# Performance work log

Measured on AMD Instinct MI355X. Metric: run time of the kernel, lower is better.

Reference implementation:

```python
import jax, jax.numpy as jnp
import numpy as np
import math

H = 1024      # hidden_size
NH = 16       # num_attention_heads
HD = H // NH  # head_dim = 64
FF = 4096     # intermediate_size
AD = 256      # adapter_hidden_size
NB = 320      # num_buckets
MAXD = 800    # max_bucket_distance
B = 4
S = 1024
EPS = 1e-5


def _rel_bucket(rel):
    # HF WavLM _relative_positions_bucket
    nb = NB // 2
    buckets = (rel > 0).astype(jnp.int32) * nb
    rel = jnp.abs(rel)
    max_exact = nb // 2
    is_small = rel < max_exact
    large = max_exact + (
        jnp.log(jnp.maximum(rel, 1).astype(jnp.float32) / max_exact)
        / math.log(MAXD / max_exact) * (nb - max_exact)
    ).astype(jnp.int32)
    large = jnp.minimum(large, nb - 1)
    return buckets + jnp.where(is_small, rel, large)


def _ln(x, g, b):
    m = x.mean(-1, keepdims=True)
    v = ((x - m) ** 2).mean(-1, keepdims=True)
    return (x - m) * jax.lax.rsqrt(v + EPS) * g + b


def setup_inputs() -> dict:
    key = jax.random.key(0)
    ks = jax.random.split(key, 12)
    sc = 0.02
    w = lambda k, shape: jax.random.normal(k, shape, jnp.float32) * sc
    return dict(
        x=jax.random.normal(ks[0], (B, S, H), jnp.float32),
        Wq=w(ks[1], (H, H)), bq=jnp.zeros((H,), jnp.float32),
        Wk=w(ks[2], (H, H)), bk=jnp.zeros((H,), jnp.float32),
        Wv=w(ks[3], (H, H)), bv=jnp.zeros((H,), jnp.float32),
        Wo=w(ks[4], (H, H)), bo=jnp.zeros((H,), jnp.float32),
        Wg=w(ks[5], (8, HD)), bg=jnp.zeros((8,), jnp.float32),
        gru_const=jnp.ones((1, NH, 1, 1), jnp.float32),
        rel_embed=w(ks[6], (NB, NH)),
        ln1_g=jnp.ones((H,), jnp.float32), ln1_b=jnp.zeros((H,), jnp.float32),
        W1=w(ks[7], (FF, H)), b1=jnp.zeros((FF,), jnp.float32),
        W2=w(ks[8], (H, FF)), b2=jnp.zeros((H,), jnp.float32),
        ln2_g=jnp.ones((H,), jnp.float32), ln2_b=jnp.zeros((H,), jnp.float32),
        Wad=w(ks[9], (AD, H)), bad=jnp.zeros((AD,), jnp.float32),
        Wau=w(ks[10], (H, AD)), bau=jnp.zeros((H,), jnp.float32),
    )


def reference(x, Wq, bq, Wk, bk, Wv, bv, Wo, bo, Wg, bg, gru_const, rel_embed,
              ln1_g, ln1_b, W1, b1, W2, b2, ln2_g, ln2_b, Wad, bad, Wau, bau):
    b, s, _ = x.shape
    # --- relative position bias (first layer: position_bias=None) ---
    pos = jnp.arange(s)
    rel = pos[None, :] - pos[:, None]                 # memory - context
    pos_bias = rel_embed[_rel_bucket(rel)].transpose(2, 0, 1)  # (nh, s, s)

    # --- GRU-style gating of the bias (per batch, head, query pos) ---
    xh = x.reshape(b, s, NH, HD).transpose(0, 2, 1, 3)         # (b, nh, s, hd)
    gproj = jnp.einsum('bhsd,ed->bhse', xh, Wg) + bg           # (b, nh, s, 8)
    gproj = gproj.reshape(b, NH, s, 2, 4).sum(-1)              # (b, nh, s, 2)
    gate = jax.nn.sigmoid(gproj)
    gate_a, gate_b = gate[..., 0:1], gate[..., 1:2]            # (b, nh, s, 1)
    gate_out = gate_a * (gate_b * gru_const - 1.0) + 2.0       # (b, nh, s, 1)
    gated_bias = gate_out * pos_bias[None]                     # (b, nh, s, s)

    # --- multi-head self-attention with additive gated bias ---
    q = (x @ Wq.T + bq).reshape(b, s, NH, HD)
    k = (x @ Wk.T + bk).reshape(b, s, NH, HD)
    v = (x @ Wv.T + bv).reshape(b, s, NH, HD)
    scores = jnp.einsum('bihd,bjhd->bhij', q, k) * (HD ** -0.5) + gated_bias
    attn = jax.nn.softmax(scores, axis=-1)
    ctx = jnp.einsum('bhij,bjhd->bihd', attn, v).reshape(b, s, H)
    attn_out = ctx @ Wo.T + bo

    # --- residual + LN, FFN + adapter (idx_without_adapter=None path) + LN ---
    h = _ln(x + attn_out, ln1_g, ln1_b)
    ff = jax.nn.gelu(h @ W1.T + b1, approximate=False) @ W2.T + b2
    adapt = jax.nn.elu(h @ Wad.T + bad) @ Wau.T + bau
    h = h + ff + adapt
    return _ln(h, ln2_g, ln2_b)
```

## Files before the change

### kernel.cpp

```cpp
#include <hip/hip_runtime.h>
#include <cmath>

typedef unsigned short u16;
using short8 = __attribute__((ext_vector_type(8))) short;
using f32x4  = __attribute__((ext_vector_type(4))) float;

__device__ __forceinline__ u16 f2bf(float f) {
  union { float f; unsigned u; } c; c.f = f;
  unsigned r = c.u + 0x7fffu + ((c.u >> 16) & 1u);
  return (u16)(r >> 16);
}
__device__ __forceinline__ float bf2f(u16 b) {
  union { unsigned u; float f; } c; c.u = ((unsigned)b) << 16;
  return c.f;
}

__device__ __forceinline__ void gld_lds16(void* lds, const void* g) {
  __builtin_amdgcn_global_load_lds(
      (const __attribute__((address_space(1))) void*)g,
      (__attribute__((address_space(3))) void*)lds, 16, 0, 0);
}

__global__ __launch_bounds__(256) void cvt_bf16(const float* __restrict__ in,
                                                u16* __restrict__ out, int n4) {
  int i = blockIdx.x * 256 + threadIdx.x;
  if (i >= n4) return;
  float4 v = ((const float4*)in)[i];
  ushort4 o;
  o.x = f2bf(v.x); o.y = f2bf(v.y); o.z = f2bf(v.z); o.w = f2bf(v.w);
  ((ushort4*)out)[i] = o;
}

__global__ __launch_bounds__(256) void btab_kernel(const float* __restrict__ rel_embed,
                                                   float* __restrict__ btab) {
  int idx = blockIdx.x * 256 + threadIdx.x;
  if (idx >= 16 * 2048) return;
  int h = idx >> 11;
  int d = idx & 2047;
  if (d >= 2047) return;
  int rel = d - 1023;
  int bucket = (rel > 0) ? 160 : 0;
  int ar = rel < 0 ? -rel : rel;
  if (ar < 80) {
    bucket += ar;
  } else {
    int large = 80 + (int)(logf((float)ar / 80.0f) / 2.3025851f * 80.0f);
    if (large > 159) large = 159;
    bucket += large;
  }
  btab[h * 2048 + d] = rel_embed[bucket * 16 + h];
}

__global__ __launch_bounds__(256) void gate_kernel(const float* __restrict__ x,
                                                   const float* __restrict__ Wg,
                                                   const float* __restrict__ bg,
                                                   const float* __restrict__ gc,
                                                   float* __restrict__ gate_out) {
  int gw = blockIdx.x * 4 + (threadIdx.x >> 6);
  int lane = threadIdx.x & 63;
  int s = gw & 1023, bh = gw >> 10, b = bh >> 4, h = bh & 15;
  float wA = Wg[lane] + Wg[64 + lane] + Wg[128 + lane] + Wg[192 + lane];
  float wB = Wg[256 + lane] + Wg[320 + lane] + Wg[384 + lane] + Wg[448 + lane];
  float xv = x[((size_t)(b * 1024 + s)) * 1024 + h * 64 + lane];
  float pa = xv * wA, pb = xv * wB;
  #pragma unroll
  for (int m = 1; m < 64; m <<= 1) {
    pa += __shfl_xor(pa, m, 64);
    pb += __shfl_xor(pb, m, 64);
  }
  if (lane == 0) {
    float bgA = bg[0] + bg[1] + bg[2] + bg[3];
    float bgB = bg[4] + bg[5] + bg[6] + bg[7];
    float ga = 1.f / (1.f + expf(-(pa + bgA)));
    float gb = 1.f / (1.f + expf(-(pb + bgB)));
    gate_out[(size_t)bh * 1024 + s] = ga * (gb * gc[h] - 1.f) + 2.f;
  }
}

__global__ __launch_bounds__(256) void vtrans_kernel(const u16* __restrict__ vb,
                                                     u16* __restrict__ vt) {
  __shared__ u16 tile[64 * 65];
  int bh = blockIdx.y, b = bh >> 4, h = bh & 15;
  int s0 = blockIdx.x * 64;
  int tid = threadIdx.x;
  int r = tid >> 3, c = (tid & 7) * 8;
  #pragma unroll
  for (int p = 0; p < 2; ++p) {
    int s = p * 32 + r;
    uint4 vv = *(const uint4*)&vb[((size_t)(b * 1024 + s0 + s)) * 1024 + h * 64 + c];
    const u16* pv = (const u16*)&vv;
    #pragma unroll
    for (int e = 0; e < 8; ++e) tile[(c + e) * 65 + s] = pv[e];
  }
  __syncthreads();
  int d = tid & 63, jc0 = tid >> 6;
  #pragma unroll
  for (int jc = jc0; jc < 8; jc += 4) {
    u16 tmp[8];
    #pragma unroll
    for (int e = 0; e < 8; ++e) tmp[e] = tile[d * 65 + jc * 8 + e];
    *(uint4*)&vt[((size_t)(bh * 64 + d)) * 1024 + s0 + jc * 8] = *(uint4*)tmp;
  }
}

template <int MODE>
__global__ __launch_bounds__(256, 3) void gemm_bt(
    const u16* __restrict__ A, const u16* __restrict__ Bw,
    int Kfull, int Ksub, int N,
    const float* __restrict__ bias0, const float* __restrict__ bias1,
    const float* __restrict__ bias2,
    float* __restrict__ outf, float* __restrict__ outf1,
    u16* __restrict__ ob0, u16* __restrict__ ob1, u16* __restrict__ ob2) {
  __shared__ __align__(16) u16 As[2][128 * 32];
  __shared__ __align__(16) u16 Bs[2][128 * 32];
  const int tid = threadIdx.x;
  const int lane = tid & 63, wave = tid >> 6;
  const int quad = lane >> 4, l16 = lane & 15;
  const int bm = blockIdx.x * 128, bn = blockIdx.y * 128;
  const int kz = blockIdx.z;
  const int k0base = kz * Ksub;
  const int nsteps = Ksub >> 5;
  const int wm = (wave & 1) * 64, wn = (wave >> 1) * 64;
  const int sr = lane & 15;
  const int skc = (lane >> 4) * 8;

  const u16* a0 = A + (size_t)(bm + wave * 32 + sr) * Kfull + k0base + skc;
  const u16* b0 = Bw + (size_t)(bn + wave * 32 + sr) * Kfull + k0base + skc;
  const size_t rstep = (size_t)16 * Kfull;

  f32x4 acc[4][4] = {};

  gld_lds16(&As[0][wave * 1024], a0);
  gld_lds16(&As[0][wave * 1024 + 512], a0 + rstep);
  gld_lds16(&Bs[0][wave * 1024], b0);
  gld_lds16(&Bs[0][wave * 1024 + 512], b0 + rstep);

  int p = 0;
  for (int ks = 0; ks < nsteps; ++ks) {
    if (ks + 1 < nsteps) {
      int ko = (ks + 1) * 32;
      gld_lds16(&As[p ^ 1][wave * 1024], a0 + ko);
      gld_lds16(&As[p ^ 1][wave * 1024 + 512], a0 + rstep + ko);
      gld_lds16(&Bs[p ^ 1][wave * 1024], b0 + ko);
      gld_lds16(&Bs[p ^ 1][wave * 1024 + 512], b0 + rstep + ko);
      asm volatile("s_waitcnt vmcnt(4)" ::: "memory");
    } else {
      asm volatile("s_waitcnt vmcnt(0)" ::: "memory");
    }
    __builtin_amdgcn_s_barrier();

    const u16* Ap = As[p];
    const u16* Bp = Bs[p];
    short8 af[4], bf[4];
    #pragma unroll
    for (int mi = 0; mi < 4; ++mi)
      af[mi] = *(const short8*)&Ap[((wm >> 4) + mi) * 512 + quad * 128 + l16 * 8];
    #pragma unroll
    for (int ni = 0; ni < 4; ++ni)
      bf[ni] = *(const short8*)&Bp[((wn >> 4) + ni) * 512 + quad * 128 + l16 * 8];
    #pragma unroll
    for (int mi = 0; mi < 4; ++mi)
      #pragma unroll
      for (int ni = 0; ni < 4; ++ni)
        acc[mi][ni] = __builtin_amdgcn_mfma_f32_16x16x32_bf16(af[mi], bf[ni], acc[mi][ni], 0, 0, 0);

    __builtin_amdgcn_s_barrier();
    p ^= 1;
  }

  float* outp = (MODE == 3) ? (kz ? outf1 : outf) : outf;

  #pragma unroll
  for (int mi = 0; mi < 4; ++mi) {
    #pragma unroll
    for (int ni = 0; ni < 4; ++ni) {
      int col = bn + wn + ni * 16 + l16;
      #pragma unroll
      for (int r = 0; r < 4; ++r) {
        int m = bm + wm + mi * 16 + quad * 4 + r;
        float v = acc[mi][ni][r];
        if constexpr (MODE == 0) {
          int seg = col >> 10;
          int nloc = col & 1023;
          const float* bs = seg == 0 ? bias0 : (seg == 1 ? bias1 : bias2);
          u16* dst = seg == 0 ? ob0 : (seg == 1 ? ob1 : ob2);
          v += bs[nloc];
          if (seg == 0) v *= 0.125f;
          dst[(size_t)m * 1024 + nloc] = f2bf(v);
        } else if constexpr (MODE == 2) {
          if (col < 4096) {
            float t = v + bias0[col];
            float g = 0.5f * t * (1.f + erff(t * 0.70710678118f));
            ob0[(size_t)m * 4096 + col] = f2bf(g);
          } else {
            int nloc = col - 4096;
            float t = v + bias1[nloc];
            float e = t > 0.f ? t : expm1f(t);
            ob1[(size_t)m * 256 + nloc] = f2bf(e);
          }
        } else if constexpr (MODE == 3) {
          outp[(size_t)m * N + col] = v;
        } else {
          outp[(size_t)m * N + col] += v;
        }
      }
    }
  }
}

__global__ __launch_bounds__(256) void attn_kernel(
    const u16* __restrict__ qb, const u16* __restrict__ kb, const u16* __restrict__ vt,
    const float* __restrict__ gate, const float* __restrict__ btab,
    u16* __restrict__ ctxb) {
  __shared__ __align__(16) u16 Qs[64 * 64];
  __shared__ __align__(16) u16 Ks[64 * 64];
  __shared__ __align__(16) u16 Vs[64 * 64];
  __shared__ __align__(16) u16 Ps[4][16 * 64];
  __shared__ u16 btl[2048];
  __shared__ float gbuf[64];

  const int tid = threadIdx.x;
  const int lane = tid & 63, wave = tid >> 6;
  const int quad = lane >> 4, l16 = lane & 15;
  const int it0 = blockIdx.x * 64;
  const int bh = blockIdx.y, b = bh >> 4, h = bh & 15;
  const int sr = lane & 15;
  const int skc = (lane >> 4) * 8;

  for (int idx = tid; idx < 2047; idx += 256) btl[idx] = f2bf(btab[h * 2048 + idx]);
  if (tid < 64) gbuf[tid] = gate[(size_t)bh * 1024 + it0 + tid];

  #pragma unroll
  for (int hf = 0; hf < 2; ++hf)
    gld_lds16(&Qs[wave * 1024 + hf * 512],
              &qb[((size_t)(b * 1024 + it0 + wave * 16 + sr)) * 1024 + h * 64 + hf * 32 + skc]);

  f32x4 oacc[4] = {};
  float mrow[4], lrow[4];
  #pragma unroll
  for (int r = 0; r < 4; ++r) { mrow[r] = -1e30f; lrow[r] = 0.f; }

  __syncthreads();

  for (int jt = 0; jt < 16; ++jt) {
    int j0 = jt * 64;
    #pragma unroll
    for (int hf = 0; hf < 2; ++hf) {
      gld_lds16(&Ks[wave * 1024 + hf * 512],
                &kb[((size_t)(b * 1024 + j0 + wave * 16 + sr)) * 1024 + h * 64 + hf * 32 + skc]);
      gld_lds16(&Vs[wave * 1024 + hf * 512],
                &vt[((size_t)(bh * 64 + wave * 16 + sr)) * 1024 + j0 + hf * 32 + skc]);
    }
    __syncthreads();

    f32x4 sacc[4] = {};
    #pragma unroll
    for (int c = 0; c < 2; ++c) {
      short8 aq = *(const short8*)&Qs[wave * 1024 + (c * 4 + quad) * 128 + l16 * 8];
      #pragma unroll
      for (int nt = 0; nt < 4; ++nt) {
        short8 bk8 = *(const short8*)&Ks[nt * 1024 + (c * 4 + quad) * 128 + l16 * 8];
        sacc[nt] = __builtin_amdgcn_mfma_f32_16x16x32_bf16(aq, bk8, sacc[nt], 0, 0, 0);
      }
    }

    float sc[4][4], mt[4];
    #pragma unroll
    for (int r = 0; r < 4; ++r) {
      int i_loc = wave * 16 + quad * 4 + r;
      int i_glob = it0 + i_loc;
      float g = gbuf[i_loc];
      float mx = -1e30f;
      #pragma unroll
      for (int nt = 0; nt < 4; ++nt) {
        int j = j0 + nt * 16 + l16;
        float s = sacc[nt][r] + g * bf2f(btl[j - i_glob + 1023]);
        sc[nt][r] = s;
        mx = fmaxf(mx, s);
      }
      mt[r] = mx;
    }
    #pragma unroll
    for (int m = 1; m < 16; m <<= 1)
      #pragma unroll
      for (int r = 0; r < 4; ++r) mt[r] = fmaxf(mt[r], __shfl_xor(mt[r], m, 64));

    float alpha[4], ls[4];
    #pragma unroll
    for (int r = 0; r < 4; ++r) {
      float mnew = fmaxf(mrow[r], mt[r]);
      alpha[r] = __expf(mrow[r] - mnew);
      mrow[r] = mnew;
      float lsum = 0.f;
      #pragma unroll
      for (int nt = 0; nt < 4; ++nt) {
        float p = __expf(sc[nt][r] - mnew);
        sc[nt][r] = p;
        lsum += p;
      }
      ls[r] = lsum;
    }
    #pragma unroll
    for (int m = 1; m < 16; m <<= 1)
      #pragma unroll
      for (int r = 0; r < 4; ++r) ls[r] += __shfl_xor(ls[r], m, 64);
    #pragma unroll
    for (int r = 0; r < 4; ++r) lrow[r] = lrow[r] * alpha[r] + ls[r];

    #pragma unroll
    for (int nt = 0; nt < 4; ++nt)
      #pragma unroll
      for (int r = 0; r < 4; ++r)
        Ps[wave][(nt * 2 + (l16 >> 3)) * 128 + (quad * 4 + r) * 8 + (l16 & 7)] = f2bf(sc[nt][r]);

    #pragma unroll
    for (int dt = 0; dt < 4; ++dt)
      #pragma unroll
      for (int r = 0; r < 4; ++r) oacc[dt][r] *= alpha[r];

    #pragma unroll
    for (int c = 0; c < 2; ++c) {
      short8 ap = *(const short8*)&Ps[wave][(c * 4 + quad) * 128 + l16 * 8];
      #pragma unroll
      for (int dt = 0; dt < 4; ++dt) {
        short8 bv8 = *(const short8*)&Vs[dt * 1024 + (c * 4 + quad) * 128 + l16 * 8];
        oacc[dt] = __builtin_amdgcn_mfma_f32_16x16x32_bf16(ap, bv8, oacc[dt], 0, 0, 0);
      }
    }
    __syncthreads();
  }

  #pragma unroll
  for (int dt = 0; dt < 4; ++dt)
    #pragma unroll
    for (int r = 0; r < 4; ++r) {
      int i_loc = wave * 16 + quad * 4 + r;
      int d = dt * 16 + l16;
      float o = oacc[dt][r] / lrow[r];
      ctxb[((size_t)(b * 1024 + it0 + i_loc)) * 1024 + h * 64 + d] = f2bf(o);
    }
}

template <bool WRITE_BF16, bool TWO_BIAS>
__global__ __launch_bounds__(256) void redln_kernel(
    const float* __restrict__ p0, const float* __restrict__ p1,
    const float* __restrict__ extra, const float* __restrict__ bias,
    const float* __restrict__ bias2,
    const float* __restrict__ g, const float* __restrict__ bta,
    float* __restrict__ outf, u16* __restrict__ outb) {
  __shared__ float red[8];
  int row = blockIdx.x, tid = threadIdx.x;
  int lane = tid & 63, wave = tid >> 6;
  size_t base = (size_t)row * 1024 + tid * 4;
  float4 a = *(const float4*)&p0[base];
  float4 bb = *(const float4*)&p1[base];
  float4 c = *(const float4*)&extra[base];
  float4 d = *(const float4*)&bias[tid * 4];
  float4 v;
  v.x = a.x + bb.x + c.x + d.x;
  v.y = a.y + bb.y + c.y + d.y;
  v.z = a.z + bb.z + c.z + d.z;
  v.w = a.w + bb.w + c.w + d.w;
  if (TWO_BIAS) {
    float4 d2 = *(const float4*)&bias2[tid * 4];
    v.x += d2.x; v.y += d2.y; v.z += d2.z; v.w += d2.w;
  }
  float s = v.x + v.y + v.z + v.w;
  #pragma unroll
  for (int m = 1; m < 64; m <<= 1) s += __shfl_xor(s, m, 64);
  if (lane == 0) red[wave] = s;
  __syncthreads();
  float mean = (red[0] + red[1] + red[2] + red[3]) * (1.f / 1024.f);
  float d0 = v.x - mean, d1 = v.y - mean, d2 = v.z - mean, d3 = v.w - mean;
  float sq = d0 * d0 + d1 * d1 + d2 * d2 + d3 * d3;
  #pragma unroll
  for (int m = 1; m < 64; m <<= 1) sq += __shfl_xor(sq, m, 64);
  if (lane == 0) red[4 + wave] = sq;
  __syncthreads();
  float var = (red[4] + red[5] + red[6] + red[7]) * (1.f / 1024.f);
  float rstd = rsqrtf(var + 1e-5f);
  float dd[4] = {d0, d1, d2, d3};
  #pragma unroll
  for (int e = 0; e < 4; ++e) {
    int cidx = tid * 4 + e;
    float val = dd[e] * rstd * g[cidx] + bta[cidx];
    outf[(size_t)row * 1024 + cidx] = val;
    if (WRITE_BF16) outb[(size_t)row * 1024 + cidx] = f2bf(val);
  }
}

extern "C" void kernel_launch(void* const* d_in, const int* in_sizes, int n_in,
                              void* d_out, int out_size, void* d_ws, size_t ws_size,
                              hipStream_t stream) {
  const float* x    = (const float*)d_in[0];
  const float* Wq   = (const float*)d_in[1];  const float* bq  = (const float*)d_in[2];
  const float* Wk   = (const float*)d_in[3];  const float* bk  = (const float*)d_in[4];
  const float* Wv   = (const float*)d_in[5];  const float* bv  = (const float*)d_in[6];
  const float* Wo   = (const float*)d_in[7];  const float* bo  = (const float*)d_in[8];
  const float* Wg   = (const float*)d_in[9];  const float* bg  = (const float*)d_in[10];
  const float* gc   = (const float*)d_in[11];
  const float* rel  = (const float*)d_in[12];
  const float* ln1g = (const float*)d_in[13]; const float* ln1b = (const float*)d_in[14];
  const float* W1   = (const float*)d_in[15]; const float* b1  = (const float*)d_in[16];
  const float* W2   = (const float*)d_in[17]; const float* b2  = (const float*)d_in[18];
  const float* ln2g = (const float*)d_in[19]; const float* ln2b = (const float*)d_in[20];
  const float* Wad  = (const float*)d_in[21]; const float* bad = (const float*)d_in[22];
  const float* Wau  = (const float*)d_in[23]; const float* bau = (const float*)d_in[24];
  float* out = (float*)d_out;

  char* ws = (char*)d_ws;
  const size_t MB = 1ull << 20;
  const size_t KB = 1ull << 10;
  u16*   xb   = (u16*)(ws + 0 * MB);
  u16*   wqkv = (u16*)(ws + 8 * MB);
  u16*   w1ad = (u16*)(ws + 16 * MB);
  u16*   w2b  = (u16*)(ws + 25 * MB);
  u16*   waub = (u16*)(ws + 33 * MB);
  u16*   wob  = (u16*)(ws + 34 * MB);
  u16*   qb   = (u16*)(ws + 36 * MB);
  u16*   kb   = (u16*)(ws + 44 * MB);
  u16*   vbp  = (u16*)(ws + 52 * MB);
  float* gate = (float*)(ws + 60 * MB);
  float* btab = (float*)(ws + 60 * MB + 256 * KB);
  u16*   ctxb = (u16*)(ws + 61 * MB);
  u16*   vtb  = (u16*)(ws + 69 * MB);
  float* hf   = (float*)(ws + 77 * MB);
  u16*   hb   = (u16*)(ws + 93 * MB);
  float* wop0 = (float*)(ws + 0 * MB);
  float* wop1 = (float*)(ws + 101 * MB);
  u16*   ffb  = (u16*)(ws + 36 * MB);
  u16*   adp  = (u16*)(ws + 68 * MB);
  float* p0   = (float*)(ws + 0 * MB);
  float* p1   = (float*)(ws + 101 * MB);
  (void)ws_size; (void)n_in; (void)in_sizes; (void)out_size;

  auto cvt = [&](const float* src, u16* dst, int n) {
    cvt_bf16<<<(n / 4 + 255) / 256, 256, 0, stream>>>(src, dst, n / 4);
  };
  cvt(x, xb, 4096 * 1024);
  cvt(Wq, wqkv,               1024 * 1024);
  cvt(Wk, wqkv + 1024 * 1024, 1024 * 1024);
  cvt(Wv, wqkv + 2 * 1024 * 1024, 1024 * 1024);
  cvt(Wo, wob, 1024 * 1024);
  cvt(W1, w1ad, 4096 * 1024);
  cvt(Wad, w1ad + 4096 * 1024, 256 * 1024);
  cvt(W2, w2b, 4096 * 1024);
  cvt(Wau, waub, 1024 * 256);

  btab_kernel<<<128, 256, 0, stream>>>(rel, btab);
  gate_kernel<<<16384, 256, 0, stream>>>(x, Wg, bg, gc, gate);

  gemm_bt<0><<<dim3(32, 24, 1), 256, 0, stream>>>(xb, wqkv, 1024, 1024, 3072,
      bq, bk, bv, nullptr, nullptr, qb, kb, vbp);
  vtrans_kernel<<<dim3(16, 64), 256, 0, stream>>>(vbp, vtb);
  attn_kernel<<<dim3(16, 64), 256, 0, stream>>>(qb, kb, vtb, gate, btab, ctxb);
  gemm_bt<3><<<dim3(32, 8, 2), 256, 0, stream>>>(ctxb, wob, 1024, 512, 1024,
      nullptr, nullptr, nullptr, wop0, wop1, nullptr, nullptr, nullptr);
  redln_kernel<true, false><<<4096, 256, 0, stream>>>(wop0, wop1, x, bo, nullptr,
      ln1g, ln1b, hf, hb);
  gemm_bt<2><<<dim3(32, 34, 1), 256, 0, stream>>>(hb, w1ad, 1024, 1024, 4352,
      b1, bad, nullptr, nullptr, nullptr, ffb, adp, nullptr);
  gemm_bt<3><<<dim3(32, 8, 2), 256, 0, stream>>>(ffb, w2b, 4096, 2048, 1024,
      nullptr, nullptr, nullptr, p0, p1, nullptr, nullptr, nullptr);
  gemm_bt<4><<<dim3(32, 8, 1), 256, 0, stream>>>(adp, waub, 256, 256, 1024,
      nullptr, nullptr, nullptr, p0, nullptr, nullptr, nullptr, nullptr);
  redln_kernel<false, true><<<4096, 256, 0, stream>>>(p0, p1, hf, b2, bau,
      ln2g, ln2b, out, nullptr);
}
```

Baseline: 570.5 us.

## Use 256x128 GEMM tiles with triple-buffered LDS and fuse adapter-up into FFN-down

The bf16 MFMA GEMM now uses 256x128 block tiles, with each wave computing 128x64, and a three-stage LDS pipeline that prefetches two k-steps ahead. It also drops the second barrier per iteration. The FFN-down GEMM and adapter-up GEMM are merged into one K=4352 GEMM by concatenating the GELU and ELU activations and padding W2 and Wau into one interleaved weight matrix, which removes a separate accumulate pass. Larger tiles raise arithmetic intensity but halve the grid, lower occupancy to two blocks per CU and need more registers and LDS.

```diff
diff --git a/kernel.cpp b/kernel.cpp
--- a/kernel.cpp
+++ b/kernel.cpp
@@ -29,6 +29,18 @@
   ushort4 o;
   o.x = f2bf(v.x); o.y = f2bf(v.y); o.z = f2bf(v.z); o.w = f2bf(v.w);
   ((ushort4*)out)[i] = o;
+}
+
+__global__ __launch_bounds__(256) void cvt_pad(const float* __restrict__ in,
+                                               u16* __restrict__ out,
+                                               int incols4, int outstride, int n4) {
+  int i = blockIdx.x * 256 + threadIdx.x;
+  if (i >= n4) return;
+  int row = i / incols4, c = i - row * incols4;
+  float4 v = ((const float4*)in)[i];
+  ushort4 o;
+  o.x = f2bf(v.x); o.y = f2bf(v.y); o.z = f2bf(v.z); o.w = f2bf(v.w);
+  *(ushort4*)&out[(size_t)row * outstride + c * 4] = o;
 }
 
 __global__ __launch_bounds__(256) void btab_kernel(const float* __restrict__ rel_embed,
@@ -104,80 +116,80 @@
 }
 
 template <int MODE>
-__global__ __launch_bounds__(256, 3) void gemm_bt(
+__global__ __launch_bounds__(256, 2) void gemm_bt(
     const u16* __restrict__ A, const u16* __restrict__ Bw,
-    int Kfull, int Ksub, int N,
+    int K, int Ksub, int N,
     const float* __restrict__ bias0, const float* __restrict__ bias1,
     const float* __restrict__ bias2,
-    float* __restrict__ outf, float* __restrict__ outf1,
+    float* __restrict__ outf,
     u16* __restrict__ ob0, u16* __restrict__ ob1, u16* __restrict__ ob2) {
-  __shared__ __align__(16) u16 As[2][128 * 32];
-  __shared__ __align__(16) u16 Bs[2][128 * 32];
+  __shared__ __align__(16) u16 As[3][256 * 32];
+  __shared__ __align__(16) u16 Bs[3][128 * 32];
   const int tid = threadIdx.x;
   const int lane = tid & 63, wave = tid >> 6;
   const int quad = lane >> 4, l16 = lane & 15;
-  const int bm = blockIdx.x * 128, bn = blockIdx.y * 128;
+  const int bm = blockIdx.x * 256, bn = blockIdx.y * 128;
   const int kz = blockIdx.z;
-  const int k0base = kz * Ksub;
   const int nsteps = Ksub >> 5;
-  const int wm = (wave & 1) * 64, wn = (wave >> 1) * 64;
-  const int sr = lane & 15;
-  const int skc = (lane >> 4) * 8;
-
-  const u16* a0 = A + (size_t)(bm + wave * 32 + sr) * Kfull + k0base + skc;
-  const u16* b0 = Bw + (size_t)(bn + wave * 32 + sr) * Kfull + k0base + skc;
-  const size_t rstep = (size_t)16 * Kfull;
-
-  f32x4 acc[4][4] = {};
-
-  gld_lds16(&As[0][wave * 1024], a0);
-  gld_lds16(&As[0][wave * 1024 + 512], a0 + rstep);
-  gld_lds16(&Bs[0][wave * 1024], b0);
-  gld_lds16(&Bs[0][wave * 1024 + 512], b0 + rstep);
-
-  int p = 0;
+  const int sr = lane & 15, skc = (lane >> 4) * 8;
+
+  const u16* a0 = A + (size_t)(bm + wave * 64 + sr) * K + kz * Ksub + skc;
+  const u16* b0 = Bw + (size_t)(bn + wave * 32 + sr) * K + kz * Ksub + skc;
+  const size_t ra = (size_t)16 * K;
+
+  f32x4 acc[8][4] = {};
+
+  #pragma unroll
+  for (int t = 0; t < 4; ++t) gld_lds16(&As[0][(wave * 4 + t) * 512], a0 + t * ra);
+  #pragma unroll
+  for (int t = 0; t < 2; ++t) gld_lds16(&Bs[0][(wave * 2 + t) * 512], b0 + t * ra);
+  if (nsteps > 1) {
+    #pragma unroll
+    for (int t = 0; t < 4; ++t) gld_lds16(&As[1][(wave * 4 + t) * 512], a0 + t * ra + 32);
+    #pragma unroll
+    for (int t = 0; t < 2; ++t) gld_lds16(&Bs[1][(wave * 2 + t) * 512], b0 + t * ra + 32);
+  }
+
+  int cur = 0, nxt2 = 2;
   for (int ks = 0; ks < nsteps; ++ks) {
-    if (ks + 1 < nsteps) {
-      int ko = (ks + 1) * 32;
-      gld_lds16(&As[p ^ 1][wave * 1024], a0 + ko);
-      gld_lds16(&As[p ^ 1][wave * 1024 + 512], a0 + rstep + ko);
-      gld_lds16(&Bs[p ^ 1][wave * 1024], b0 + ko);
-      gld_lds16(&Bs[p ^ 1][wave * 1024 + 512], b0 + rstep + ko);
-      asm volatile("s_waitcnt vmcnt(4)" ::: "memory");
-    } else {
-      asm volatile("s_waitcnt vmcnt(0)" ::: "memory");
-    }
+    if (ks + 1 < nsteps) asm volatile("s_waitcnt vmcnt(6)" ::: "memory");
+    else                 asm volatile("s_waitcnt vmcnt(0)" ::: "memory");
     __builtin_amdgcn_s_barrier();
-
-    const u16* Ap = As[p];
-    const u16* Bp = Bs[p];
-    short8 af[4], bf[4];
-    #pragma unroll
-    for (int mi = 0; mi < 4; ++mi)
-      af[mi] = *(const short8*)&Ap[((wm >> 4) + mi) * 512 + quad * 128 + l16 * 8];
+    if (ks + 2 < nsteps) {
+      int ko = (ks + 2) * 32;
+      #pragma unroll
+      for (int t = 0; t < 4; ++t) gld_lds16(&As[nxt2][(wave * 4 + t) * 512], a0 + t * ra + ko);
+      #pragma unroll
+      for (int t = 0; t < 2; ++t) gld_lds16(&Bs[nxt2][(wave * 2 + t) * 512], b0 + t * ra + ko);
+    }
+    const u16* Ap = As[cur];
+    const u16* Bp = Bs[cur];
+    short8 af[8], bf[4];
+    #pragma unroll
+    for (int mi = 0; mi < 8; ++mi)
+      af[mi] = *(const short8*)&Ap[((wave & 1) * 8 + mi) * 512 + quad * 128 + l16 * 8];
     #pragma unroll
     for (int ni = 0; ni < 4; ++ni)
-      bf[ni] = *(const short8*)&Bp[((wn >> 4) + ni) * 512 + quad * 128 + l16 * 8];
-    #pragma unroll
-    for (int mi = 0; mi < 4; ++mi)
+      bf[ni] = *(const short8*)&Bp[((wave >> 1) * 4 + ni) * 512 + quad * 128 + l16 * 8];
+    #pragma unroll
+    for (int mi = 0; mi < 8; ++mi)
       #pragma unroll
       for (int ni = 0; ni < 4; ++ni)
         acc[mi][ni] = __builtin_amdgcn_mfma_f32_16x16x32_bf16(af[mi], bf[ni], acc[mi][ni], 0, 0, 0);
-
-    __builtin_amdgcn_s_barrier();
-    p ^= 1;
-  }
-
-  float* outp = (MODE == 3) ? (kz ? outf1 : outf) : outf;
-
-  #pragma unroll
-  for (int mi = 0; mi < 4; ++mi) {
+    cur = (cur == 2) ? 0 : cur + 1;
+    nxt2 = (nxt2 == 2) ? 0 : nxt2 + 1;
+  }
+
+  float* outp = outf + (size_t)kz * 4194304;
+
+  #pragma unroll
+  for (int mi = 0; mi < 8; ++mi) {
     #pragma unroll
     for (int ni = 0; ni < 4; ++ni) {
-      int col = bn + wn + ni * 16 + l16;
+      int col = bn + (wave >> 1) * 64 + ni * 16 + l16;
       #pragma unroll
       for (int r = 0; r < 4; ++r) {
-        int m = bm + wm + mi * 16 + quad * 4 + r;
+        int m = bm + (wave & 1) * 128 + mi * 16 + quad * 4 + r;
         float v = acc[mi][ni][r];
         if constexpr (MODE == 0) {
           int seg = col >> 10;
@@ -191,17 +203,14 @@
           if (col < 4096) {
             float t = v + bias0[col];
             float g = 0.5f * t * (1.f + erff(t * 0.70710678118f));
-            ob0[(size_t)m * 4096 + col] = f2bf(g);
+            ob0[(size_t)m * 4352 + col] = f2bf(g);
           } else {
-            int nloc = col - 4096;
-            float t = v + bias1[nloc];
+            float t = v + bias1[col - 4096];
             float e = t > 0.f ? t : expm1f(t);
-            ob1[(size_t)m * 256 + nloc] = f2bf(e);
+            ob0[(size_t)m * 4352 + col] = f2bf(e);
           }
-        } else if constexpr (MODE == 3) {
+        } else {
           outp[(size_t)m * N + col] = v;
-        } else {
-          outp[(size_t)m * N + col] += v;
         }
       }
     }
@@ -411,27 +420,23 @@
   char* ws = (char*)d_ws;
   const size_t MB = 1ull << 20;
   const size_t KB = 1ull << 10;
-  u16*   xb   = (u16*)(ws + 0 * MB);
-  u16*   wqkv = (u16*)(ws + 8 * MB);
-  u16*   w1ad = (u16*)(ws + 16 * MB);
-  u16*   w2b  = (u16*)(ws + 25 * MB);
-  u16*   waub = (u16*)(ws + 33 * MB);
-  u16*   wob  = (u16*)(ws + 34 * MB);
-  u16*   qb   = (u16*)(ws + 36 * MB);
-  u16*   kb   = (u16*)(ws + 44 * MB);
-  u16*   vbp  = (u16*)(ws + 52 * MB);
-  float* gate = (float*)(ws + 60 * MB);
-  float* btab = (float*)(ws + 60 * MB + 256 * KB);
-  u16*   ctxb = (u16*)(ws + 61 * MB);
-  u16*   vtb  = (u16*)(ws + 69 * MB);
-  float* hf   = (float*)(ws + 77 * MB);
-  u16*   hb   = (u16*)(ws + 93 * MB);
-  float* wop0 = (float*)(ws + 0 * MB);
-  float* wop1 = (float*)(ws + 101 * MB);
-  u16*   ffb  = (u16*)(ws + 36 * MB);
-  u16*   adp  = (u16*)(ws + 68 * MB);
-  float* p0   = (float*)(ws + 0 * MB);
-  float* p1   = (float*)(ws + 101 * MB);
+  u16*   xb    = (u16*)(ws + 0 * MB);
+  u16*   wqkv  = (u16*)(ws + 8 * MB);
+  u16*   qb    = (u16*)(ws + 14 * MB);
+  u16*   kb    = (u16*)(ws + 22 * MB);
+  u16*   vbp   = (u16*)(ws + 30 * MB);
+  u16*   vtb   = (u16*)(ws + 38 * MB);
+  float* gate  = (float*)(ws + 46 * MB);
+  float* btab  = (float*)(ws + 46 * MB + 256 * KB);
+  u16*   ffadp = (u16*)(ws + 0 * MB);
+  float* P0    = (float*)(ws + 34 * MB);
+  float* P1    = (float*)(ws + 50 * MB);
+  u16*   ctxb  = (u16*)(ws + 66 * MB);
+  u16*   wob   = (u16*)(ws + 74 * MB);
+  u16*   w1ad  = (u16*)(ws + 76 * MB);
+  u16*   w2au  = (u16*)(ws + 85 * MB);
+  float* hf    = (float*)(ws + 94 * MB);
+  u16*   hb    = (u16*)(ws + 110 * MB);
   (void)ws_size; (void)n_in; (void)in_sizes; (void)out_size;
 
   auto cvt = [&](const float* src, u16* dst, int n) {
@@ -444,26 +449,24 @@
   cvt(Wo, wob, 1024 * 1024);
   cvt(W1, w1ad, 4096 * 1024);
   cvt(Wad, w1ad + 4096 * 1024, 256 * 1024);
-  cvt(W2, w2b, 4096 * 1024);
-  cvt(Wau, waub, 1024 * 256);
+  cvt_pad<<<(1024 * 1024 + 255) / 256, 256, 0, stream>>>(W2, w2au, 1024, 4352, 1024 * 1024);
+  cvt_pad<<<(64 * 1024 + 255) / 256, 256, 0, stream>>>(Wau, w2au + 4096, 64, 4352, 64 * 1024);
 
   btab_kernel<<<128, 256, 0, stream>>>(rel, btab);
   gate_kernel<<<16384, 256, 0, stream>>>(x, Wg, bg, gc, gate);
 
-  gemm_bt<0><<<dim3(32, 24, 1), 256, 0, stream>>>(xb, wqkv, 1024, 1024, 3072,
-      bq, bk, bv, nullptr, nullptr, qb, kb, vbp);
+  gemm_bt<0><<<dim3(16, 24, 1), 256, 0, stream>>>(xb, wqkv, 1024, 1024, 3072,
+      bq, bk, bv, nullptr, qb, kb, vbp);
   vtrans_kernel<<<dim3(16, 64), 256, 0, stream>>>(vbp, vtb);
   attn_kernel<<<dim3(16, 64), 256, 0, stream>>>(qb, kb, vtb, gate, btab, ctxb);
-  gemm_bt<3><<<dim3(32, 8, 2), 256, 0, stream>>>(ctxb, wob, 1024, 512, 1024,
-      nullptr, nullptr, nullptr, wop0, wop1, nullptr, nullptr, nullptr);
-  redln_kernel<true, false><<<4096, 256, 0, stream>>>(wop0, wop1, x, bo, nullptr,
+  gemm_bt<3><<<dim3(16, 8, 2), 256, 0, stream>>>(ctxb, wob, 1024, 512, 1024,
+      nullptr, nullptr, nullptr, P0, nullptr, nullptr, nullptr);
+  redln_kernel<true, false><<<4096, 256, 0, stream>>>(P0, P1, x, bo, nullptr,
       ln1g, ln1b, hf, hb);
-  gemm_bt<2><<<dim3(32, 34, 1), 256, 0, stream>>>(hb, w1ad, 1024, 1024, 4352,
-      b1, bad, nullptr, nullptr, nullptr, ffb, adp, nullptr);
-  gemm_bt<3><<<dim3(32, 8, 2), 256, 0, stream>>>(ffb, w2b, 4096, 2048, 1024,
-      nullptr, nullptr, nullptr, p0, p1, nullptr, nullptr, nullptr);
-  gemm_bt<4><<<dim3(32, 8, 1), 256, 0, stream>>>(adp, waub, 256, 256, 1024,
-      nullptr, nullptr, nullptr, p0, nullptr, nullptr, nullptr, nullptr);
-  redln_kernel<false, true><<<4096, 256, 0, stream>>>(p0, p1, hf, b2, bau,
+  gemm_bt<2><<<dim3(16, 34, 1), 256, 0, stream>>>(hb, w1ad, 1024, 1024, 4352,
+      b1, bad, nullptr, nullptr, ffadp, nullptr, nullptr);
+  gemm_bt<3><<<dim3(16, 8, 2), 256, 0, stream>>>(ffadp, w2au, 4352, 2176, 1024,
+      nullptr, nullptr, nullptr, P0, nullptr, nullptr, nullptr);
+  redln_kernel<false, true><<<4096, 256, 0, stream>>>(P0, P1, hf, b2, bau,
       ln2g, ln2b, out, nullptr);
 }
```

Result: slower. 621.5 us (+8.9%).
